# Performance work log

Measured on AMD Instinct MI355X. Metric: run time of the kernel, lower is better.

Reference implementation:

```python
import jax, jax.numpy as jnp
import numpy as np
import math

N = 50000      # nodes
E = 800000     # edges
IN = 256       # in_dim
HD = 128       # n_hid
T = 3          # num_types
R = 4          # num_relations
NH = 8         # n_heads
DK = HD // NH  # d_k = 16
L = 2          # n_layers
MAXT = 240     # RTE max_len


def _rte_table():
    # Faithful to the torch code (including its precedence: (10000**arange)/n_hid/2,
    # which overflows to inf for large indices -> div_term -> 0).
    pos = jnp.arange(MAXT, dtype=jnp.float32)[:, None]
    div = 1.0 / (10000.0 ** jnp.arange(0.0, HD * 2, 2.0, dtype=jnp.float32) / HD / 2.0)
    emb = jnp.zeros((MAXT, HD * 2), jnp.float32)
    emb = emb.at[:, 0::2].set(jnp.sin(pos * div) / math.sqrt(HD))
    emb = emb.at[:, 1::2].set(jnp.cos(pos * div) / math.sqrt(HD))
    return emb


def setup_inputs() -> dict:
    key = jax.random.key(0)
    ks = jax.random.split(key, 20)
    s = 0.02
    inp = {}
    inp["node_feature"] = jax.random.normal(ks[0], (N, IN), jnp.float32)
    inp["node_type"] = jax.random.randint(ks[1], (N,), 0, T)
    inp["edge_time"] = jax.random.randint(ks[2], (E,), 0, MAXT)
    inp["edge_type"] = jax.random.randint(ks[3], (E,), 0, R)
    inp["edge_index"] = jax.random.randint(ks[4], (2, E), 0, N)
    # adapt layer (per node type)
    inp["adapt_W"] = jax.random.normal(ks[5], (T, IN, HD), jnp.float32) * s
    inp["adapt_b"] = jax.random.normal(ks[6], (T, HD), jnp.float32) * s
    # per-layer, per-type linears (stored as [in,out] so y = x @ W + b)
    inp["Wk"] = jax.random.normal(ks[7], (L, T, HD, HD), jnp.float32) * s
    inp["bk"] = jnp.zeros((L, T, HD), jnp.float32)
    inp["Wq"] = jax.random.normal(ks[8], (L, T, HD, HD), jnp.float32) * s
    inp["bq"] = jnp.zeros((L, T, HD), jnp.float32)
    inp["Wv"] = jax.random.normal(ks[9], (L, T, HD, HD), jnp.float32) * s
    inp["bv"] = jnp.zeros((L, T, HD), jnp.float32)
    inp["Wa"] = jax.random.normal(ks[10], (L, T, HD, HD), jnp.float32) * s
    inp["ba"] = jnp.zeros((L, T, HD), jnp.float32)
    inp["rel_pri"] = jnp.ones((L, T, R, T, NH), jnp.float32)
    glorot = math.sqrt(6.0 / (DK + DK))
    inp["rel_att"] = jax.random.uniform(ks[11], (L, R, NH, DK, DK), jnp.float32, -glorot, glorot)
    inp["rel_msg"] = jax.random.uniform(ks[12], (L, R, NH, DK, DK), jnp.float32, -glorot, glorot)
    inp["skip"] = jnp.ones((L, T), jnp.float32)
    inp["rte_emb"] = _rte_table()                                   # [240, 2*HD], frozen sinusoid
    inp["rte_W"] = jax.random.normal(ks[13], (L, HD * 2, HD), jnp.float32) * s
    inp["rte_b"] = jnp.zeros((L, HD), jnp.float32)
    return inp


def _per_type_linear(x, types, W, b):
    # x:[M,in], types:[M] in [0,T); W:[T,in,out], b:[T,out]
    out = jnp.zeros((x.shape[0], W.shape[-1]), x.dtype)
    for t in range(W.shape[0]):
        out = jnp.where((types == t)[:, None], x @ W[t] + b[t], out)
    return out


def _segment_softmax(s, seg, n):
    # s:[E,H] softmax over edges sharing the same target node
    m = jax.ops.segment_max(s, seg, num_segments=n)
    e = jnp.exp(s - m[seg])
    z = jax.ops.segment_sum(e, seg, num_segments=n)
    return e / z[seg]


def _forward(node_feature, node_type, edge_time, edge_type, edge_index,
             adapt_W, adapt_b, Wk, bk, Wq, bq, Wv, bv, Wa, ba,
             rel_pri, rel_att, rel_msg, skip, rte_emb, rte_W, rte_b):
    src = edge_index[0]  # j (source)
    dst = edge_index[1]  # i (target)
    st = node_type[src]
    tt = node_type[dst]
    rel1h = jax.nn.one_hot(edge_type, R, dtype=node_feature.dtype)  # [E,R]

    x = jnp.tanh(_per_type_linear(node_feature, node_type, adapt_W, adapt_b))  # [N,HD]

    for l in range(L):
        # relative temporal encoding of source features (per edge)
        rte = rte_emb[edge_time] @ rte_W[l] + rte_b[l]          # [E,HD]
        src_vec = x[src] + rte                                   # [E,HD]
        # q is a pure function of target node features -> compute per node, gather
        q_nodes = _per_type_linear(x, node_type, Wq[l], bq[l])   # [N,HD]
        q = q_nodes[dst].reshape(E, NH, DK)
        k = _per_type_linear(src_vec, st, Wk[l], bk[l]).reshape(E, NH, DK)
        v = _per_type_linear(src_vec, st, Wv[l], bv[l]).reshape(E, NH, DK)
        k = jnp.einsum('ehd,er,rhdk->ehk', k, rel1h, rel_att[l])
        v = jnp.einsum('ehd,er,rhdk->ehk', v, rel1h, rel_msg[l])
        pri = rel_pri[l][tt, edge_type, st]                      # [E,NH]
        score = (q * k).sum(-1) * pri / math.sqrt(DK)            # [E,NH]
        att = _segment_softmax(score, dst, N)                    # [E,NH]
        msg = (v * att[..., None]).reshape(E, HD)                # [E,HD]
        aggr = jax.ops.segment_sum(msg, dst, num_segments=N)     # [N,HD]
        aggr = jax.nn.gelu(aggr, approximate=False)
        out = _per_type_linear(aggr, node_type, Wa[l], ba[l])    # [N,HD]
        alpha = jax.nn.sigmoid(skip[l])[node_type][:, None]      # [N,1]
        x = out * alpha + x * (1.0 - alpha)
    return x


def reference(node_feature, node_type, edge_time, edge_type, edge_index,
              adapt_W, adapt_b, Wk, bk, Wq, bq, Wv, bv, Wa, ba,
              rel_pri, rel_att, rel_msg, skip, rte_emb, rte_W, rte_b):
    return _forward(node_feature, node_type, edge_time, edge_type, edge_index,
                    adapt_W, adapt_b, Wk, bk, Wq, bq, Wv, bv, Wa, ba,
                    rel_pri, rel_att, rel_msg, skip, rte_emb, rte_W, rte_b)
```

## Files before the change

kernel.cpp:

```cpp
#include <hip/hip_runtime.h>
#include <cstdint>
#include <cstddef>


namespace {

constexpr int T_N  = 3;
constexpr int R_N  = 4;
constexpr int HD   = 128;
constexpr int IND  = 256;
constexpr int NH   = 8;
constexpr int MAXT = 240;

typedef unsigned short u16;
typedef unsigned int   u32;
typedef _Float16 f16;
typedef __attribute__((ext_vector_type(8))) _Float16 f16x8;
typedef __attribute__((ext_vector_type(4))) float    f32x4;

__global__ void k_fill_i32(int* __restrict__ p, int v, int n) {
  int i = blockIdx.x * 256 + threadIdx.x;
  if (i < n) p[i] = v;
}
__global__ void k_copy_i32(int* __restrict__ d, const int* __restrict__ s, int n) {
  int i = blockIdx.x * 256 + threadIdx.x;
  if (i < n) d[i] = s[i];
}
__global__ void k_hist_dst(const int* __restrict__ dst, int* __restrict__ cnt, int E) {
  int i = blockIdx.x * 256 + threadIdx.x;
  if (i < E) atomicAdd(&cnt[dst[i]], 1);
}
__global__ void k_scan_a(const int* __restrict__ in, int* __restrict__ out,
                         int* __restrict__ bsums, int n) {
  __shared__ int s[256];
  int gid = blockIdx.x * 256 + threadIdx.x;
  int v = (gid < n) ? in[gid] : 0;
  s[threadIdx.x] = v;
  __syncthreads();
  for (int off = 1; off < 256; off <<= 1) {
    int t = (threadIdx.x >= off) ? s[threadIdx.x - off] : 0;
    __syncthreads();
    s[threadIdx.x] += t;
    __syncthreads();
  }
  if (gid < n) out[gid] = s[threadIdx.x] - v;
  if (threadIdx.x == 255) bsums[blockIdx.x] = s[255];
}
__global__ void k_scan_b(int* __restrict__ bsums, int nb) {
  __shared__ int s[256];
  int v = (threadIdx.x < nb) ? bsums[threadIdx.x] : 0;
  s[threadIdx.x] = v;
  __syncthreads();
  for (int off = 1; off < 256; off <<= 1) {
    int t = (threadIdx.x >= off) ? s[threadIdx.x - off] : 0;
    __syncthreads();
    s[threadIdx.x] += t;
    __syncthreads();
  }
  if (threadIdx.x < nb) bsums[threadIdx.x] = s[threadIdx.x] - v;
}
__global__ void k_scan_c(int* __restrict__ out, const int* __restrict__ bsums, int n) {
  int gid = blockIdx.x * 256 + threadIdx.x;
  if (gid < n) out[gid] += bsums[blockIdx.x];
}
__global__ void k_rank_dst(const int* __restrict__ dst, int* __restrict__ cur,
                           int* __restrict__ rank, int E) {
  int i = blockIdx.x * 256 + threadIdx.x;
  if (i < E) rank[i] = atomicAdd(&cur[dst[i]], 1);
}
__global__ void k_bhist(const int* __restrict__ src, const int* __restrict__ etype,
                        const int* __restrict__ ntype, int* __restrict__ bcnt, int E) {
  __shared__ int loc[12];
  if (threadIdx.x < 12) loc[threadIdx.x] = 0;
  __syncthreads();
  int i = blockIdx.x * 256 + threadIdx.x;
  if (i < E) {
    int b = ntype[src[i]] * R_N + etype[i];
    atomicAdd(&loc[b], 1);
  }
  __syncthreads();
  if (threadIdx.x < 12) atomicAdd(&bcnt[threadIdx.x], loc[threadIdx.x]);
}
__global__ void k_bscan(const int* __restrict__ bcnt, int* __restrict__ bal,
                        int* __restrict__ bcur) {
  if (threadIdx.x == 0 && blockIdx.x == 0) {
    int run = 0;
    for (int b = 0; b < 12; b++) {
      bal[b] = run;
      bcur[b] = run;
      run += (bcnt[b] + 63) & ~63;
    }
    bal[12] = run;
  }
}
__global__ void k_bscatter(const int* __restrict__ src, const int* __restrict__ etype,
                           const int* __restrict__ ntype, int* __restrict__ bcur,
                           int* __restrict__ esorted, int E) {
  __shared__ int loc[12];
  __shared__ int base[12];
  if (threadIdx.x < 12) loc[threadIdx.x] = 0;
  __syncthreads();
  int i = blockIdx.x * 256 + threadIdx.x;
  int b = 0, lpos = 0;
  if (i < E) {
    b = ntype[src[i]] * R_N + etype[i];
    lpos = atomicAdd(&loc[b], 1);
  }
  __syncthreads();
  if (threadIdx.x < 12) {
    int c = loc[threadIdx.x];
    base[threadIdx.x] = (c > 0) ? atomicAdd(&bcur[threadIdx.x], c) : 0;
  }
  __syncthreads();
  if (i < E) esorted[base[b] + lpos] = i;
}
__global__ void k_nhist(const int* __restrict__ ntype, int* __restrict__ ncnt, int N) {
  __shared__ int loc[3];
  if (threadIdx.x < 3) loc[threadIdx.x] = 0;
  __syncthreads();
  int i = blockIdx.x * 256 + threadIdx.x;
  if (i < N) atomicAdd(&loc[ntype[i]], 1);
  __syncthreads();
  if (threadIdx.x < 3) atomicAdd(&ncnt[threadIdx.x], loc[threadIdx.x]);
}
__global__ void k_nscan(const int* __restrict__ ncnt, int* __restrict__ nal,
                        int* __restrict__ ncur) {
  if (threadIdx.x == 0 && blockIdx.x == 0) {
    int run = 0;
    for (int t = 0; t < 3; t++) {
      nal[t] = run;
      ncur[t] = run;
      run += (ncnt[t] + 63) & ~63;
    }
    nal[3] = run;
  }
}
__global__ void k_nscatter(const int* __restrict__ ntype, int* __restrict__ ncur,
                           int* __restrict__ nsorted, int N) {
  __shared__ int loc[3];
  __shared__ int base[3];
  if (threadIdx.x < 3) loc[threadIdx.x] = 0;
  __syncthreads();
  int i = blockIdx.x * 256 + threadIdx.x;
  int t = 0, lpos = 0;
  if (i < N) {
    t = ntype[i];
    lpos = atomicAdd(&loc[t], 1);
  }
  __syncthreads();
  if (threadIdx.x < 3) {
    int c = loc[threadIdx.x];
    base[threadIdx.x] = (c > 0) ? atomicAdd(&ncur[threadIdx.x], c) : 0;
  }
  __syncthreads();
  if (i < N) nsorted[base[t] + lpos] = i;
}

__global__ void k_transp(const float* __restrict__ src, u16* __restrict__ dst,
                         int Kd, int Cd) {
  int c = blockIdx.x;
  int t = blockIdx.y;
  for (int k = threadIdx.x; k < Kd; k += blockDim.x)
    dst[((size_t)t * Cd + c) * Kd + k] =
        __builtin_bit_cast(u16, (f16)src[((size_t)t * Kd + k) * Cd + c]);
}

__global__ void k_rte(const float* __restrict__ emb, const float* __restrict__ W,
                      const float* __restrict__ bias, u16* __restrict__ out, int l) {
  int t = blockIdx.x;
  int lane = threadIdx.x;
  __shared__ __align__(16) float s[2 * HD];
  ((float4*)s)[lane] = ((const float4*)(emb + (size_t)t * 2 * HD))[lane];
  __syncthreads();
  const float* Wl = W + (size_t)l * 2 * HD * HD;
  float o0 = bias[l * HD + 2 * lane];
  float o1 = bias[l * HD + 2 * lane + 1];
  #pragma unroll 4
  for (int k = 0; k < 2 * HD; k++) {
    float xv = s[k];
    float2 w = ((const float2*)(Wl + (size_t)k * HD))[lane];
    o0 = fmaf(xv, w.x, o0);
    o1 = fmaf(xv, w.y, o1);
  }
  u32 pk = (u32)__builtin_bit_cast(u16, (f16)o0)
         | ((u32)__builtin_bit_cast(u16, (f16)o1) << 16);
  ((u32*)out)[t * 64 + lane] = pk;
}

__global__ void k_wcomb(const float* __restrict__ Wk, const float* __restrict__ Wv,
                        const float* __restrict__ bk, const float* __restrict__ bv,
                        const float* __restrict__ Ratt, const float* __restrict__ Rmsg,
                        u16* __restrict__ Wcomb, float* __restrict__ bcomb, int l) {
  int bc = blockIdx.x;
  int b  = bc >> 8;
  int c  = bc & 255;
  int st = b >> 2, rt = b & 3;
  int k  = threadIdx.x;
  bool isv = (c >= HD);
  int c0 = isv ? c - HD : c;
  int h  = c0 >> 4, cc = c0 & 15;
  const float* W = (isv ? Wv : Wk) + (((size_t)(l * T_N + st) * HD) + k) * HD + h * 16;
  const float* A = (isv ? Rmsg : Ratt) + (((size_t)(l * R_N + rt) * NH + h) * 16) * 16 + cc;
  float s = 0.f;
  #pragma unroll
  for (int d = 0; d < 16; d++) s = fmaf(W[d], A[d * 16], s);
  Wcomb[((size_t)b * 256 + c) * HD + k] = __builtin_bit_cast(u16, (f16)s);
  if (k == 0) {
    const float* bb = (isv ? bv : bk) + (size_t)(l * T_N + st) * HD + h * 16;
    float sb = 0.f;
    #pragma unroll
    for (int d = 0; d < 16; d++) sb = fmaf(bb[d], A[d * 16], sb);
    bcomb[b * 256 + c] = sb;
  }
}

template<int K, int ACT, bool AHALF>
__global__ __launch_bounds__(256) void k_ngemm(
    const float* __restrict__ Af, const u16* __restrict__ Ah,
    const u16* __restrict__ WT, const float* __restrict__ bias,
    const int* __restrict__ nsorted, const int* __restrict__ nal,
    const float* __restrict__ skip_l,
    float* __restrict__ out_f, u16* __restrict__ out_h,
    const float* __restrict__ xin) {
  int tile0 = blockIdx.x * 64;
  if (tile0 >= nal[3]) return;
  int t = 0;
  #pragma unroll
  for (int i = 1; i < 3; i++) t += (tile0 >= nal[i]);

  __shared__ __align__(16) u16 ab[64 * K];
  __shared__ int s_nid[64];
  int tid = threadIdx.x;
  int lane = tid & 63, w = tid >> 6;
  int l15 = lane & 15, l4 = lane >> 4;

  if (tid < 64) s_nid[tid] = nsorted[tile0 + tid];
  __syncthreads();

  {
    int r = tid >> 2, q4 = tid & 3;
    int nid = s_nid[r];
    char* rowp = (char*)ab + r * (2 * K);
    int sw = (r & 7) << 4;
    int base = q4 * (K / 2);
    if (nid >= 0) {
      if (AHALF) {
        const f16x8* ap = (const f16x8*)(Ah + (size_t)nid * K + q4 * (K / 4));
        #pragma unroll
        for (int i = 0; i < K / 32; i++)
          *(f16x8*)(rowp + ((base + 16 * i) ^ sw)) = ap[i];
      } else {
        const float4* ap = (const float4*)(Af + (size_t)nid * K + q4 * (K / 4));
        #pragma unroll
        for (int i = 0; i < K / 32; i++) {
          float4 a = ap[2 * i], a2 = ap[2 * i + 1];
          f16x8 hv;
          hv[0] = (f16)a.x;  hv[1] = (f16)a.y;  hv[2] = (f16)a.z;  hv[3] = (f16)a.w;
          hv[4] = (f16)a2.x; hv[5] = (f16)a2.y; hv[6] = (f16)a2.z; hv[7] = (f16)a2.w;
          *(f16x8*)(rowp + ((base + 16 * i) ^ sw)) = hv;
        }
      }
    } else {
      f16x8 z;
      #pragma unroll
      for (int j = 0; j < 8; j++) z[j] = (f16)0.f;
      #pragma unroll
      for (int i = 0; i < K / 32; i++)
        *(f16x8*)(rowp + ((base + 16 * i) ^ sw)) = z;
    }
  }
  __syncthreads();

  f32x4 acc[4][2];
  #pragma unroll
  for (int ni = 0; ni < 2; ni++) {
    float bc = bias[t * HD + w * 32 + ni * 16 + l15];
    #pragma unroll
    for (int mi = 0; mi < 4; mi++) {
      acc[mi][ni][0] = bc; acc[mi][ni][1] = bc;
      acc[mi][ni][2] = bc; acc[mi][ni][3] = bc;
    }
  }
  const u16* Wt = WT + (size_t)t * HD * K;
  #pragma unroll
  for (int ks = 0; ks < K / 32; ks++) {
    int k0 = ks * 32 + 8 * l4;
    f16x8 bf[2], af[4];
    #pragma unroll
    for (int ni = 0; ni < 2; ni++)
      bf[ni] = *(const f16x8*)(Wt + (size_t)(w * 32 + ni * 16 + l15) * K + k0);
    #pragma unroll
    for (int mi = 0; mi < 4; mi++) {
      int row = mi * 16 + l15;
      af[mi] = *(const f16x8*)((const char*)ab + row * (2 * K) +
                               ((2 * k0) ^ ((row & 7) << 4)));
    }
    #pragma unroll
    for (int mi = 0; mi < 4; mi++)
      #pragma unroll
      for (int ni = 0; ni < 2; ni++)
        acc[mi][ni] = __builtin_amdgcn_mfma_f32_16x16x32_f16(af[mi], bf[ni],
                                                             acc[mi][ni], 0, 0, 0);
  }

  float alpha = 0.f;
  if (ACT == 2) alpha = 1.f / (1.f + expf(-skip_l[t]));
  #pragma unroll
  for (int mi = 0; mi < 4; mi++)
    #pragma unroll
    for (int r = 0; r < 4; r++) {
      int rowl = mi * 16 + l4 * 4 + r;
      int nid = s_nid[rowl];
      if (nid >= 0) {
        #pragma unroll
        for (int ni = 0; ni < 2; ni++) {
          int c = w * 32 + ni * 16 + l15;
          float val = acc[mi][ni][r];
          if (ACT == 0) val = tanhf(val);
          if (ACT == 2) {
            float xo = xin[(size_t)nid * HD + c];
            val = val * alpha + xo * (1.f - alpha);
          }
          if (out_f) out_f[(size_t)nid * HD + c] = val;
          if (out_h) out_h[(size_t)nid * HD + c] =
              __builtin_bit_cast(u16, (f16)val);
        }
      }
    }
}

__global__ __launch_bounds__(256) void k_edge_gemm(
    const u16* __restrict__ x_h, const u16* __restrict__ rte_h,
    const u16* __restrict__ Wcomb, const float* __restrict__ bcomb,
    const u16* __restrict__ q_h, const int* __restrict__ esorted,
    const int* __restrict__ bal, const int* __restrict__ src,
    const int* __restrict__ dst, const int* __restrict__ etime,
    const int* __restrict__ ntype, const int* __restrict__ rank,
    const float* __restrict__ pri_l,
    u16* __restrict__ score_h, u16* __restrict__ v_csr) {
  int tile0 = blockIdx.x * 64;
  if (tile0 >= bal[12]) return;
  int b = 0;
  #pragma unroll
  for (int i = 1; i < 12; i++) b += (tile0 >= bal[i]);
  int st = b >> 2, rt = b & 3;

  __shared__ __align__(16) u16 albuf[64 * HD];
  __shared__ int s_eid[64];
  __shared__ int s_dst[64];
  __shared__ int s_rank[64];
  int tid = threadIdx.x;
  int lane = tid & 63, w = tid >> 6;
  int l15 = lane & 15, l4 = lane >> 4;

  if (tid < 64) {
    int e = esorted[tile0 + tid];
    s_eid[tid] = e;
    s_dst[tid] = (e >= 0) ? dst[e] : 0;
    s_rank[tid] = (e >= 0) ? rank[e] : 0;
  }
  __syncthreads();

  {
    int r = tid >> 2, qq = tid & 3;
    int e = s_eid[r];
    char* rowp = (char*)albuf + r * 256;
    int sw = (r & 7) << 4;
    if (e >= 0) {
      const f16x8* xs = (const f16x8*)(x_h + (size_t)src[e] * HD + qq * 32);
      const f16x8* rp = (const f16x8*)(rte_h + (size_t)etime[e] * HD + qq * 32);
      #pragma unroll
      for (int i = 0; i < 4; i++) {
        f16x8 hv = xs[i] + rp[i];
        *(f16x8*)(rowp + ((qq * 64 + i * 16) ^ sw)) = hv;
      }
    } else {
      f16x8 z;
      #pragma unroll
      for (int j = 0; j < 8; j++) z[j] = (f16)0.f;
      #pragma unroll
      for (int i = 0; i < 4; i++)
        *(f16x8*)(rowp + ((qq * 64 + i * 16) ^ sw)) = z;
    }
  }
  __syncthreads();

  f32x4 acc[4][4];
  #pragma unroll
  for (int ni = 0; ni < 4; ni++) {
    float bc = bcomb[b * 256 + w * 64 + ni * 16 + l15];
    #pragma unroll
    for (int mi = 0; mi < 4; mi++) {
      acc[mi][ni][0] = bc; acc[mi][ni][1] = bc;
      acc[mi][ni][2] = bc; acc[mi][ni][3] = bc;
    }
  }
  const u16* Wb = Wcomb + (size_t)b * 256 * HD;
  #pragma unroll
  for (int ks = 0; ks < 4; ks++) {
    int k0 = ks * 32 + 8 * l4;
    f16x8 bf[4], af[4];
    #pragma unroll
    for (int ni = 0; ni < 4; ni++)
      bf[ni] = *(const f16x8*)(Wb + (size_t)(w * 64 + ni * 16 + l15) * HD + k0);
    #pragma unroll
    for (int mi = 0; mi < 4; mi++) {
      int row = mi * 16 + l15;
      af[mi] = *(const f16x8*)((const char*)albuf + row * 256 +
                               ((2 * k0) ^ ((row & 7) << 4)));
    }
    #pragma unroll
    for (int mi = 0; mi < 4; mi++)
      #pragma unroll
      for (int ni = 0; ni < 4; ni++)
        acc[mi][ni] = __builtin_amdgcn_mfma_f32_16x16x32_f16(af[mi], bf[ni],
                                                             acc[mi][ni], 0, 0, 0);
  }
  __syncthreads();

  if (w < 2) {
    #pragma unroll
    for (int mi = 0; mi < 4; mi++)
      #pragma unroll
      for (int r = 0; r < 4; r++) {
        int row = mi * 16 + l4 * 4 + r;
        char* rowp = (char*)albuf + row * 256;
        int sw = (row & 7) << 4;
        #pragma unroll
        for (int ni = 0; ni < 4; ni++) {
          int c = w * 64 + ni * 16 + l15;
          *(u16*)(rowp + ((2 * c) ^ sw)) =
              __builtin_bit_cast(u16, (f16)acc[mi][ni][r]);
        }
      }
  } else {
    int wv = w - 2;
    #pragma unroll
    for (int mi = 0; mi < 4; mi++)
      #pragma unroll
      for (int r = 0; r < 4; r++) {
        int rowl = mi * 16 + l4 * 4 + r;
        if (s_eid[rowl] >= 0) {
          u16* vp = v_csr + (size_t)s_rank[rowl] * HD + wv * 64 + l15;
          #pragma unroll
          for (int ni = 0; ni < 4; ni++)
            vp[ni * 16] = __builtin_bit_cast(u16, (f16)acc[mi][ni][r]);
        }
      }
  }
  __syncthreads();

  #pragma unroll
  for (int s = 0; s < 2; s++) {
    int p = tid + 256 * s;
    int e = p >> 3, h = p & 7;
    if (s_eid[e] >= 0) {
      int d = s_dst[e];
      int tt = ntype[d];
      const char* rowp = (const char*)albuf + e * 256;
      int sw = (e & 7) << 4;
      f16x8 kh0 = *(const f16x8*)(rowp + ((h * 32) ^ sw));
      f16x8 kh1 = *(const f16x8*)(rowp + ((h * 32 + 16) ^ sw));
      const f16x8* qp = (const f16x8*)(q_h + (size_t)d * HD + h * 16);
      f16x8 qa = qp[0], qb = qp[1];
      float sc = 0.f;
      #pragma unroll
      for (int j = 0; j < 8; j++) sc += (float)qa[j] * (float)kh0[j];
      #pragma unroll
      for (int j = 0; j < 8; j++) sc += (float)qb[j] * (float)kh1[j];
      float pri = pri_l[((tt * R_N + rt) * T_N + st) * NH + h];
      score_h[(size_t)s_rank[e] * NH + h] =
          __builtin_bit_cast(u16, (f16)(sc * pri * 0.25f));
    }
  }
}

__global__ void k_aggr(const int* __restrict__ row_ptr,
                       const u16* __restrict__ score_h,
                       const u16* __restrict__ v_csr,
                       u16* __restrict__ g_h, int N) {
  int n = blockIdx.x;
  int lane = threadIdx.x;
  int start = row_ptr[n], end = row_ptr[n + 1];

  int h = lane & 7, jj = lane >> 3;
  float m = -3.0e38f;
  for (int idx = start + jj; idx < end; idx += 8)
    m = fmaxf(m, (float)__builtin_bit_cast(f16, score_h[(size_t)idx * NH + h]));
  #pragma unroll
  for (int off = 8; off < 64; off <<= 1) m = fmaxf(m, __shfl_xor(m, off));
  float z = 0.f;
  for (int idx = start + jj; idx < end; idx += 8)
    z += expf((float)__builtin_bit_cast(f16, score_h[(size_t)idx * NH + h]) - m);
  #pragma unroll
  for (int off = 8; off < 64; off <<= 1) z += __shfl_xor(z, off);

  int myh = lane >> 3;
  float md = __shfl(m, myh);
  float zd = __shfl(z, myh);
  float rz = (zd > 0.f) ? 1.f / zd : 0.f;

  float a0 = 0.f, a1 = 0.f;
  for (int idx = start; idx < end; idx++) {
    float sc = (float)__builtin_bit_cast(f16, score_h[(size_t)idx * NH + myh]);
    float wgt = expf(sc - md) * rz;
    u32 v2 = ((const u32*)(v_csr + (size_t)idx * HD))[lane];
    float v0 = (float)__builtin_bit_cast(f16, (u16)(v2 & 0xffffu));
    float v1 = (float)__builtin_bit_cast(f16, (u16)(v2 >> 16));
    a0 = fmaf(wgt, v0, a0);
    a1 = fmaf(wgt, v1, a1);
  }

  a0 = 0.5f * a0 * (1.f + erff(a0 * 0.7071067811865475f));
  a1 = 0.5f * a1 * (1.f + erff(a1 * 0.7071067811865475f));
  u32 pk = (u32)__builtin_bit_cast(u16, (f16)a0)
         | ((u32)__builtin_bit_cast(u16, (f16)a1) << 16);
  ((u32*)(g_h + (size_t)n * HD))[lane] = pk;
}

}

extern "C" void kernel_launch(void* const* d_in, const int* in_sizes, int n_in,
                              void* d_out, int out_size, void* d_ws, size_t ws_size,
                              hipStream_t stream) {
  const float* node_feature = (const float*)d_in[0];
  const int*   node_type    = (const int*)d_in[1];
  const int*   edge_time    = (const int*)d_in[2];
  const int*   edge_type    = (const int*)d_in[3];
  const int*   edge_index   = (const int*)d_in[4];
  const float* adapt_W      = (const float*)d_in[5];
  const float* adapt_b      = (const float*)d_in[6];
  const float* Wk           = (const float*)d_in[7];
  const float* bk           = (const float*)d_in[8];
  const float* Wq           = (const float*)d_in[9];
  const float* bq           = (const float*)d_in[10];
  const float* Wv           = (const float*)d_in[11];
  const float* bv           = (const float*)d_in[12];
  const float* Wa           = (const float*)d_in[13];
  const float* ba           = (const float*)d_in[14];
  const float* rel_pri      = (const float*)d_in[15];
  const float* rel_att      = (const float*)d_in[16];
  const float* rel_msg      = (const float*)d_in[17];
  const float* skip         = (const float*)d_in[18];
  const float* rte_emb      = (const float*)d_in[19];
  const float* rte_W        = (const float*)d_in[20];
  const float* rte_b        = (const float*)d_in[21];

  const int N = in_sizes[1];
  const int E = in_sizes[2];
  const int* src  = edge_index;
  const int* dstp = edge_index + E;

  float* x = (float*)d_out;

  size_t off = 0;
  auto carve = [&](size_t bytes) -> void* {
    void* p = (char*)d_ws + off;
    off += (bytes + 255) & ~(size_t)255;
    return p;
  };
  u16*   v_csr   = (u16*)  carve((size_t)E * HD * 2);
  u16*   score_h = (u16*)  carve((size_t)E * NH * 2);
  u16*   x_h     = (u16*)  carve((size_t)N * HD * 2);
  u16*   qg      = (u16*)  carve((size_t)N * HD * 2);
  u16*   rte_h   = (u16*)  carve((size_t)MAXT * HD * 2);
  u16*   Wcomb   = (u16*)  carve((size_t)12 * 256 * HD * 2);
  float* bcomb   = (float*)carve((size_t)12 * 256 * 4);
  u16*   adaptWT = (u16*)  carve((size_t)T_N * HD * IND * 2);
  u16*   WqT     = (u16*)  carve((size_t)2 * T_N * HD * HD * 2);
  u16*   WaT     = (u16*)  carve((size_t)2 * T_N * HD * HD * 2);
  int*   row_ptr = (int*)  carve((size_t)(N + 1) * 4);
  int*   cnt     = (int*)  carve((size_t)(N + 1) * 4);
  int*   rank    = (int*)  carve((size_t)E * 4);
  int*   bsums   = (int*)  carve(1024 * 4);
  int*   bcnt    = (int*)  carve(16 * 4);
  int*   bal     = (int*)  carve(16 * 4);
  int*   bcur    = (int*)  carve(16 * 4);
  int*   ncnt    = (int*)  carve(16 * 4);
  int*   nal     = (int*)  carve(16 * 4);
  int*   ncur    = (int*)  carve(16 * 4);
  const int EP = E + 12 * 64;
  const int NP = N + 3 * 64;
  int*   esorted = (int*)  carve((size_t)EP * 4);
  int*   nsorted = (int*)  carve((size_t)NP * 4);
  (void)ws_size; (void)n_in; (void)out_size;

  const int gE  = (E + 255) / 256;
  const int gN1 = (N + 1 + 255) / 256;
  const int gN  = (N + 255) / 256;
  const int gEP = (EP + 255) / 256;
  const int gNP = (NP + 255) / 256;
  const int etiles = (EP + 63) / 64;
  const int ntiles = (NP + 63) / 64;

  k_fill_i32<<<gN1, 256, 0, stream>>>(cnt, 0, N + 1);
  k_hist_dst<<<gE, 256, 0, stream>>>(dstp, cnt, E);
  k_scan_a<<<gN1, 256, 0, stream>>>(cnt, row_ptr, bsums, N + 1);
  k_scan_b<<<1, 256, 0, stream>>>(bsums, gN1);
  k_scan_c<<<gN1, 256, 0, stream>>>(row_ptr, bsums, N + 1);
  k_copy_i32<<<gN, 256, 0, stream>>>(cnt, row_ptr, N);
  k_rank_dst<<<gE, 256, 0, stream>>>(dstp, cnt, rank, E);

  k_fill_i32<<<1, 256, 0, stream>>>(bcnt, 0, 16);
  k_bhist<<<gE, 256, 0, stream>>>(src, edge_type, node_type, bcnt, E);
  k_bscan<<<1, 64, 0, stream>>>(bcnt, bal, bcur);
  k_fill_i32<<<gEP, 256, 0, stream>>>(esorted, -1, EP);
  k_bscatter<<<gE, 256, 0, stream>>>(src, edge_type, node_type, bcur, esorted, E);

  k_fill_i32<<<1, 256, 0, stream>>>(ncnt, 0, 16);
  k_nhist<<<gN, 256, 0, stream>>>(node_type, ncnt, N);
  k_nscan<<<1, 64, 0, stream>>>(ncnt, nal, ncur);
  k_fill_i32<<<gNP, 256, 0, stream>>>(nsorted, -1, NP);
  k_nscatter<<<gN, 256, 0, stream>>>(node_type, ncur, nsorted, N);

  k_transp<<<dim3(HD, T_N), 128, 0, stream>>>(adapt_W, adaptWT, IND, HD);
  for (int l = 0; l < 2; l++) {
    k_transp<<<dim3(HD, T_N), 128, 0, stream>>>(
        Wq + (size_t)l * T_N * HD * HD, WqT + (size_t)l * T_N * HD * HD, HD, HD);
    k_transp<<<dim3(HD, T_N), 128, 0, stream>>>(
        Wa + (size_t)l * T_N * HD * HD, WaT + (size_t)l * T_N * HD * HD, HD, HD);
  }

  k_ngemm<IND, 0, false><<<ntiles, 256, 0, stream>>>(
      node_feature, nullptr, adaptWT, adapt_b, nsorted, nal, nullptr,
      x, x_h, nullptr);

  for (int l = 0; l < 2; l++) {
    k_rte<<<MAXT, 64, 0, stream>>>(rte_emb, rte_W, rte_b, rte_h, l);
    k_wcomb<<<12 * 256, 128, 0, stream>>>(Wk, Wv, bk, bv, rel_att, rel_msg,
                                          Wcomb, bcomb, l);
    k_ngemm<HD, 1, true><<<ntiles, 256, 0, stream>>>(
        nullptr, x_h, WqT + (size_t)l * T_N * HD * HD, bq + (size_t)l * T_N * HD,
        nsorted, nal, nullptr, nullptr, qg, nullptr);
    k_edge_gemm<<<etiles, 256, 0, stream>>>(x_h, rte_h, Wcomb, bcomb, qg,
                                            esorted, bal, src, dstp, edge_time,
                                            node_type, rank,
                                            rel_pri + (size_t)l * T_N * R_N * T_N * NH,
                                            score_h, v_csr);
    k_aggr<<<N, 64, 0, stream>>>(row_ptr, score_h, v_csr, qg, N);
    k_ngemm<HD, 2, true><<<ntiles, 256, 0, stream>>>(
        nullptr, qg, WaT + (size_t)l * T_N * HD * HD, ba + (size_t)l * T_N * HD,
        nsorted, nal, skip + (size_t)l * T_N, x, x_h, x);
  }
}
```

Before: 934.3 us.

## Sort edges by (bucket, dst) key and remap edge-gemm tiles per XCD

Replaces the per-bucket scatter with a counting sort on the composite key (src type, relation, dst). A 600k-entry histogram and a two-level scan, carved from the v_csr buffer, order edges by destination within each bucket, so gathers and writes in the edge GEMM become more local. The edge GEMM block index is also remapped so each XCD handles a contiguous range of tiles, improving L2 locality. The cost is several extra scan launches and a larger histogram fill and scan.

Measured after the change: 960.4 us. 2.8% more time.

```diff
diff --git a/kernel.cpp b/kernel.cpp
--- a/kernel.cpp
+++ b/kernel.cpp
@@ -68,51 +68,39 @@
   int i = blockIdx.x * 256 + threadIdx.x;
   if (i < E) rank[i] = atomicAdd(&cur[dst[i]], 1);
 }
-__global__ void k_bhist(const int* __restrict__ src, const int* __restrict__ etype,
-                        const int* __restrict__ ntype, int* __restrict__ bcnt, int E) {
-  __shared__ int loc[12];
-  if (threadIdx.x < 12) loc[threadIdx.x] = 0;
-  __syncthreads();
-  int i = blockIdx.x * 256 + threadIdx.x;
-  if (i < E) {
-    int b = ntype[src[i]] * R_N + etype[i];
-    atomicAdd(&loc[b], 1);
-  }
-  __syncthreads();
-  if (threadIdx.x < 12) atomicAdd(&bcnt[threadIdx.x], loc[threadIdx.x]);
-}
-__global__ void k_bscan(const int* __restrict__ bcnt, int* __restrict__ bal,
-                        int* __restrict__ bcur) {
+__global__ void k_keyhist(const int* __restrict__ src, const int* __restrict__ etype,
+                          const int* __restrict__ ntype, const int* __restrict__ dst,
+                          int* __restrict__ hist, int N, int E) {
+  int e = blockIdx.x * 256 + threadIdx.x;
+  if (e < E) {
+    int b = ntype[src[e]] * R_N + etype[e];
+    atomicAdd(&hist[b * N + dst[e]], 1);
+  }
+}
+__global__ void k_bstart(const int* __restrict__ scan, int N, int E,
+                         int* __restrict__ bst, int* __restrict__ bal) {
   if (threadIdx.x == 0 && blockIdx.x == 0) {
+    for (int b = 0; b < 12; b++) bst[b] = scan[(size_t)b * N];
+    bst[12] = E;
     int run = 0;
     for (int b = 0; b < 12; b++) {
       bal[b] = run;
-      bcur[b] = run;
-      run += (bcnt[b] + 63) & ~63;
+      run += ((bst[b + 1] - bst[b]) + 63) & ~63;
     }
     bal[12] = run;
   }
 }
-__global__ void k_bscatter(const int* __restrict__ src, const int* __restrict__ etype,
-                           const int* __restrict__ ntype, int* __restrict__ bcur,
-                           int* __restrict__ esorted, int E) {
-  __shared__ int loc[12];
-  __shared__ int base[12];
-  if (threadIdx.x < 12) loc[threadIdx.x] = 0;
-  __syncthreads();
-  int i = blockIdx.x * 256 + threadIdx.x;
-  int b = 0, lpos = 0;
-  if (i < E) {
-    b = ntype[src[i]] * R_N + etype[i];
-    lpos = atomicAdd(&loc[b], 1);
-  }
-  __syncthreads();
-  if (threadIdx.x < 12) {
-    int c = loc[threadIdx.x];
-    base[threadIdx.x] = (c > 0) ? atomicAdd(&bcur[threadIdx.x], c) : 0;
-  }
-  __syncthreads();
-  if (i < E) esorted[base[b] + lpos] = i;
+__global__ void k_ksort(const int* __restrict__ src, const int* __restrict__ etype,
+                        const int* __restrict__ ntype, const int* __restrict__ dst,
+                        int* __restrict__ cur, const int* __restrict__ bst,
+                        const int* __restrict__ bal, int* __restrict__ esorted,
+                        int N, int E) {
+  int e = blockIdx.x * 256 + threadIdx.x;
+  if (e < E) {
+    int b = ntype[src[e]] * R_N + etype[e];
+    int p = atomicAdd(&cur[b * N + dst[e]], 1);
+    esorted[bal[b] + (p - bst[b])] = e;
+  }
 }
 __global__ void k_nhist(const int* __restrict__ ntype, int* __restrict__ ncnt, int N) {
   __shared__ int loc[3];
@@ -338,7 +326,12 @@
     const int* __restrict__ ntype, const int* __restrict__ rank,
     const float* __restrict__ pri_l,
     u16* __restrict__ score_h, u16* __restrict__ v_csr) {
-  int tile0 = blockIdx.x * 64;
+  int nt = gridDim.x;
+  int qc = nt >> 3, rc = nt & 7;
+  int xcd = blockIdx.x & 7, idx = blockIdx.x >> 3;
+  int tile = (xcd < rc) ? xcd * (qc + 1) + idx
+                        : rc * (qc + 1) + (xcd - rc) * qc + idx;
+  int tile0 = tile * 64;
   if (tile0 >= bal[12]) return;
   int b = 0;
   #pragma unroll
@@ -573,9 +566,8 @@
   int*   cnt     = (int*)  carve((size_t)(N + 1) * 4);
   int*   rank    = (int*)  carve((size_t)E * 4);
   int*   bsums   = (int*)  carve(1024 * 4);
-  int*   bcnt    = (int*)  carve(16 * 4);
+  int*   bst     = (int*)  carve(16 * 4);
   int*   bal     = (int*)  carve(16 * 4);
-  int*   bcur    = (int*)  carve(16 * 4);
   int*   ncnt    = (int*)  carve(16 * 4);
   int*   nal     = (int*)  carve(16 * 4);
   int*   ncur    = (int*)  carve(16 * 4);
@@ -585,11 +577,20 @@
   int*   nsorted = (int*)  carve((size_t)NP * 4);
   (void)ws_size; (void)n_in; (void)out_size;
 
+  const int M = 12 * N;
+  int* hist600 = (int*)v_csr;
+  int* scan600 = hist600 + ((M + 63) & ~63);
+  int* bsA     = scan600 + ((M + 63) & ~63);
+  int* bsA2    = bsA + 2560;
+  int* bsB     = bsA2 + 2560;
+
   const int gE  = (E + 255) / 256;
   const int gN1 = (N + 1 + 255) / 256;
   const int gN  = (N + 255) / 256;
   const int gEP = (EP + 255) / 256;
   const int gNP = (NP + 255) / 256;
+  const int gM  = (M + 255) / 256;
+  const int gM2 = (gM + 255) / 256;
   const int etiles = (EP + 63) / 64;
   const int ntiles = (NP + 63) / 64;
 
@@ -601,11 +602,18 @@
   k_copy_i32<<<gN, 256, 0, stream>>>(cnt, row_ptr, N);
   k_rank_dst<<<gE, 256, 0, stream>>>(dstp, cnt, rank, E);
 
-  k_fill_i32<<<1, 256, 0, stream>>>(bcnt, 0, 16);
-  k_bhist<<<gE, 256, 0, stream>>>(src, edge_type, node_type, bcnt, E);
-  k_bscan<<<1, 64, 0, stream>>>(bcnt, bal, bcur);
+  k_fill_i32<<<gM, 256, 0, stream>>>(hist600, 0, M);
+  k_keyhist<<<gE, 256, 0, stream>>>(src, edge_type, node_type, dstp,
+                                    hist600, N, E);
+  k_scan_a<<<gM, 256, 0, stream>>>(hist600, scan600, bsA, M);
+  k_scan_a<<<gM2, 256, 0, stream>>>(bsA, bsA2, bsB, gM);
+  k_scan_b<<<1, 256, 0, stream>>>(bsB, gM2);
+  k_scan_c<<<gM2, 256, 0, stream>>>(bsA2, bsB, gM);
+  k_scan_c<<<gM, 256, 0, stream>>>(scan600, bsA2, M);
+  k_bstart<<<1, 64, 0, stream>>>(scan600, N, E, bst, bal);
   k_fill_i32<<<gEP, 256, 0, stream>>>(esorted, -1, EP);
-  k_bscatter<<<gE, 256, 0, stream>>>(src, edge_type, node_type, bcur, esorted, E);
+  k_ksort<<<gE, 256, 0, stream>>>(src, edge_type, node_type, dstp,
+                                  scan600, bst, bal, esorted, N, E);
 
   k_fill_i32<<<1, 256, 0, stream>>>(ncnt, 0, 16);
   k_nhist<<<gN, 256, 0, stream>>>(node_type, ncnt, N);
```
